# Kernel tuning notes

Hardware: AMD Instinct MI355X
Metric: run time of the kernel (lower is better)

The kernel has to match this reference:

```python
import jax, jax.numpy as jnp
import numpy as np

GRID = 7
COORD = 5.0
NO_OBJ = 0.5


def _corners(xywh, r, c):
    # xywh: [...,4] with (x_cell, y_cell, w, h); r,c broadcastable grid indices
    x, y, w, h = xywh[..., 0], xywh[..., 1], xywh[..., 2], xywh[..., 3]
    cx = (x + c) / GRID
    cy = (y + r) / GRID
    return cx - w / 2, cy - h / 2, cx + w / 2, cy + h / 2


def _iou(a, b):
    ax1, ay1, ax2, ay2 = a
    bx1, by1, bx2, by2 = b
    iw = jnp.maximum(jnp.minimum(ax2, bx2) - jnp.maximum(ax1, bx1), 0.0)
    ih = jnp.maximum(jnp.minimum(ay2, by2) - jnp.maximum(ay1, by1), 0.0)
    inter = iw * ih
    area_a = (ax2 - ax1) * (ay2 - ay1)
    area_b = (bx2 - bx1) * (by2 - by1)
    union = area_a + area_b - inter
    return jnp.where(union > 0, inter / jnp.where(union > 0, union, 1.0), 0.0)


def setup_inputs() -> dict:
    key = jax.random.key(0)
    k1, k2, k3 = jax.random.split(key, 3)
    B = 8192
    data = jax.random.uniform(k1, (B, GRID, GRID, 30), dtype=jnp.float32)
    labels = jax.random.uniform(k2, (B, GRID, GRID, 30), dtype=jnp.float32)
    # obj flag at channel 4 must be exactly 1 for obj cells
    obj = jax.random.randint(k3, (B, GRID, GRID), 0, 2).astype(jnp.float32)
    labels = labels.at[..., 4].set(obj)
    return {"data": data, "labels": labels}


def reference(data, labels):
    B = data.shape[0]
    r = jnp.arange(GRID, dtype=data.dtype)[None, :, None]  # row index -> y offset
    c = jnp.arange(GRID, dtype=data.dtype)[None, None, :]  # col index -> x offset

    box1 = _corners(data[..., 0:4], r, c)
    box2 = _corners(data[..., 5:9], r, c)
    gt = _corners(labels[..., 0:4], r, c)

    iou1 = _iou(box1, gt)  # [B,7,7]
    iou2 = _iou(box2, gt)
    resp1 = iou1 >= iou2

    xy1 = jnp.sum((data[..., 0:2] - labels[..., 0:2]) ** 2, -1)
    xy2 = jnp.sum((data[..., 5:7] - labels[..., 5:7]) ** 2, -1)
    wh1 = jnp.sum((jnp.sqrt(data[..., 2:4]) - jnp.sqrt(labels[..., 2:4])) ** 2, -1)
    wh2 = jnp.sum((jnp.sqrt(data[..., 7:9]) - jnp.sqrt(labels[..., 7:9])) ** 2, -1)

    d4, d9 = data[..., 4], data[..., 9]
    co = COORD * jnp.where(resp1, xy1, xy2)
    wh = COORD * jnp.where(resp1, wh1, wh2)
    confi = jnp.where(resp1, (d4 - iou1) ** 2, (d9 - iou2) ** 2)
    noobj_in = NO_OBJ * jnp.where(resp1, d9 ** 2, d4 ** 2)
    cls = jnp.sum((data[..., 10:] - labels[..., 10:]) ** 2, -1)

    m = (labels[..., 4] == 1).astype(data.dtype)
    obj_loss = m * (co + wh + confi + noobj_in + cls)
    noobj_loss = (1.0 - m) * NO_OBJ * (d4 ** 2 + d9 ** 2)
    return jnp.sum(obj_loss + noobj_loss) / B
```

## Files before the change

### kernel.cpp

```cpp
#include <hip/hip_runtime.h>

#define COORD 5.0f
#define NO_OBJ 0.5f
#define NCELLS (8192 * 49)
#define INV_B (1.0f / 8192.0f)

#define TPB 256
#define NBLK (NCELLS / TPB)

__device__ __forceinline__ float iou_calc(float ax1, float ay1, float ax2, float ay2,
                                          float bx1, float by1, float bx2, float by2) {
    float iw = fminf(ax2, bx2) - fmaxf(ax1, bx1);
    iw = fmaxf(iw, 0.0f);
    float ih = fminf(ay2, by2) - fmaxf(ay1, by1);
    ih = fmaxf(ih, 0.0f);
    float inter = iw * ih;
    float area_a = (ax2 - ax1) * (ay2 - ay1);
    float area_b = (bx2 - bx1) * (by2 - by1);
    float uni = area_a + area_b - inter;
    return uni > 0.0f ? inter / uni : 0.0f;
}

__global__ __launch_bounds__(TPB, 4) void yolo_loss_kernel(
    const float* __restrict__ data, const float* __restrict__ labels,
    float* __restrict__ ws) {
    const int tid = threadIdx.x;
    const int idx = blockIdx.x * TPB + tid;
    const int cell = idx % 49;
    const float r = (float)(cell / 7);
    const float c = (float)(cell % 7);

    float d[30], l[30];
    const float2* dp = (const float2*)(data + (size_t)idx * 30);
    const float2* lp = (const float2*)(labels + (size_t)idx * 30);
#pragma unroll
    for (int i = 0; i < 15; i++) {
        float2 v = dp[i];
        d[2 * i] = v.x; d[2 * i + 1] = v.y;
        float2 w2 = lp[i];
        l[2 * i] = w2.x; l[2 * i + 1] = w2.y;
    }

    const float inv_g = 1.0f / 7.0f;
    float cx1 = (d[0] + c) * inv_g, cy1 = (d[1] + r) * inv_g;
    float b1x1 = cx1 - d[2] * 0.5f, b1y1 = cy1 - d[3] * 0.5f;
    float b1x2 = cx1 + d[2] * 0.5f, b1y2 = cy1 + d[3] * 0.5f;
    float cx2 = (d[5] + c) * inv_g, cy2 = (d[6] + r) * inv_g;
    float b2x1 = cx2 - d[7] * 0.5f, b2y1 = cy2 - d[8] * 0.5f;
    float b2x2 = cx2 + d[7] * 0.5f, b2y2 = cy2 + d[8] * 0.5f;
    float gx = (l[0] + c) * inv_g, gy = (l[1] + r) * inv_g;
    float gx1 = gx - l[2] * 0.5f, gy1 = gy - l[3] * 0.5f;
    float gx2 = gx + l[2] * 0.5f, gy2 = gy + l[3] * 0.5f;

    float iou1 = iou_calc(b1x1, b1y1, b1x2, b1y2, gx1, gy1, gx2, gy2);
    float iou2 = iou_calc(b2x1, b2y1, b2x2, b2y2, gx1, gy1, gx2, gy2);
    bool resp1 = iou1 >= iou2;

    float xy1 = (d[0] - l[0]) * (d[0] - l[0]) + (d[1] - l[1]) * (d[1] - l[1]);
    float xy2 = (d[5] - l[5]) * (d[5] - l[5]) + (d[6] - l[6]) * (d[6] - l[6]);
    float s2 = sqrtf(d[2]) - sqrtf(l[2]);
    float s3 = sqrtf(d[3]) - sqrtf(l[3]);
    float wh1 = s2 * s2 + s3 * s3;
    float s7 = sqrtf(d[7]) - sqrtf(l[7]);
    float s8 = sqrtf(d[8]) - sqrtf(l[8]);
    float wh2 = s7 * s7 + s8 * s8;

    float d4 = d[4], d9 = d[9];
    float co = COORD * (resp1 ? xy1 : xy2);
    float wh = COORD * (resp1 ? wh1 : wh2);
    float ci = resp1 ? (d4 - iou1) * (d4 - iou1) : (d9 - iou2) * (d9 - iou2);
    float noobj_in = NO_OBJ * (resp1 ? d9 * d9 : d4 * d4);
    float cls = 0.0f;
#pragma unroll
    for (int i = 10; i < 30; i++) {
        float t = d[i] - l[i];
        cls += t * t;
    }

    float loss = (l[4] == 1.0f)
                     ? (co + wh + ci + noobj_in + cls)
                     : NO_OBJ * (d4 * d4 + d9 * d9);
    float acc = loss * INV_B;

#pragma unroll
    for (int off = 32; off > 0; off >>= 1)
        acc += __shfl_down(acc, off, 64);

    __shared__ float wsum[4];
    if ((tid & 63) == 0) wsum[tid >> 6] = acc;
    __syncthreads();
    if (tid == 0) ws[blockIdx.x] = wsum[0] + wsum[1] + wsum[2] + wsum[3];
}

__global__ __launch_bounds__(256) void reduce_kernel(const float* __restrict__ ws,
                                                     float* __restrict__ out) {
    float s = 0.0f;
    for (int i = threadIdx.x; i < NBLK; i += 256) s += ws[i];
#pragma unroll
    for (int off = 32; off > 0; off >>= 1)
        s += __shfl_down(s, off, 64);
    __shared__ float w[4];
    if ((threadIdx.x & 63) == 0) w[threadIdx.x >> 6] = s;
    __syncthreads();
    if (threadIdx.x == 0) out[0] = w[0] + w[1] + w[2] + w[3];
}

extern "C" void kernel_launch(void* const* d_in, const int* in_sizes, int n_in,
                              void* d_out, int out_size, void* d_ws, size_t ws_size,
                              hipStream_t stream) {
    const float* data = (const float*)d_in[0];
    const float* labels = (const float*)d_in[1];
    float* out = (float*)d_out;
    float* ws = (float*)d_ws;

    yolo_loss_kernel<<<NBLK, TPB, 0, stream>>>(data, labels, ws);
    reduce_kernel<<<1, 256, 0, stream>>>(ws, out);
}
```

Measured before the change: 119.3 us.

## Stage cell tiles into LDS with double-buffered global_load_lds in persistent blocks

Replaces the one-thread-per-cell kernel, which read each cell's 30 floats with strided float2 global loads. The new kernel uses 512 persistent blocks of 128 threads that copy contiguous 128-cell tiles of data and labels into LDS with async global_load_lds, double-buffered so the next tile loads while the current one is computed. The goal is fully coalesced global traffic and overlap of loading with compute. In exchange, each block now uses about 60KB of LDS, fewer waves are resident, and the LDS reads at a stride of 30 floats may hit bank conflicts.

```diff
diff --git a/kernel.cpp b/kernel.cpp
--- a/kernel.cpp
+++ b/kernel.cpp
@@ -5,8 +5,10 @@
 #define NCELLS (8192 * 49)
 #define INV_B (1.0f / 8192.0f)
 
-#define TPB 256
-#define NBLK (NCELLS / TPB)
+#define CPB 128
+#define FPT (CPB * 30)
+#define NTILES (NCELLS / CPB)
+#define NPBLK 512
 
 __device__ __forceinline__ float iou_calc(float ax1, float ay1, float ax2, float ay2,
                                           float bx1, float by1, float bx2, float by2) {
@@ -21,18 +23,31 @@
     return uni > 0.0f ? inter / uni : 0.0f;
 }
 
-__global__ __launch_bounds__(TPB, 4) void yolo_loss_kernel(
-    const float* __restrict__ data, const float* __restrict__ labels,
-    float* __restrict__ ws) {
-    const int tid = threadIdx.x;
-    const int idx = blockIdx.x * TPB + tid;
+__device__ __forceinline__ void stage_tile(const float* __restrict__ g, float* s, int tid) {
+#pragma unroll
+    for (int j = 0; j < 7; j++) {
+        __builtin_amdgcn_global_load_lds(
+            (const __attribute__((address_space(1))) void*)(g + j * 512 + tid * 4),
+            (__attribute__((address_space(3))) void*)(s + j * 512 + tid * 4), 16, 0, 0);
+    }
+#pragma unroll
+    for (int j = 0; j < 2; j++) {
+        __builtin_amdgcn_global_load_lds(
+            (const __attribute__((address_space(1))) void*)(g + 3584 + j * 128 + tid),
+            (__attribute__((address_space(3))) void*)(s + 3584 + j * 128 + tid), 4, 0, 0);
+    }
+}
+
+__device__ __forceinline__ float cell_loss(const float* __restrict__ sd,
+                                           const float* __restrict__ sl,
+                                           int idx, int tid) {
     const int cell = idx % 49;
     const float r = (float)(cell / 7);
     const float c = (float)(cell % 7);
 
     float d[30], l[30];
-    const float2* dp = (const float2*)(data + (size_t)idx * 30);
-    const float2* lp = (const float2*)(labels + (size_t)idx * 30);
+    const float2* dp = (const float2*)(sd + tid * 30);
+    const float2* lp = (const float2*)(sl + tid * 30);
 #pragma unroll
     for (int i = 0; i < 15; i++) {
         float2 v = dp[i];
@@ -77,25 +92,49 @@
         cls += t * t;
     }
 
-    float loss = (l[4] == 1.0f)
-                     ? (co + wh + ci + noobj_in + cls)
-                     : NO_OBJ * (d4 * d4 + d9 * d9);
-    float acc = loss * INV_B;
+    return (l[4] == 1.0f) ? (co + wh + ci + noobj_in + cls)
+                          : NO_OBJ * (d4 * d4 + d9 * d9);
+}
+
+__global__ __launch_bounds__(CPB) void yolo_loss_kernel(
+    const float* __restrict__ data, const float* __restrict__ labels,
+    float* __restrict__ ws) {
+    __shared__ float sd[2][FPT];
+    __shared__ float sl[2][FPT];
+
+    const int tid = threadIdx.x;
+    float acc = 0.0f;
+    int cur = 0;
+
+    stage_tile(data + (size_t)blockIdx.x * FPT, sd[0], tid);
+    stage_tile(labels + (size_t)blockIdx.x * FPT, sl[0], tid);
+
+    for (int i = blockIdx.x; i < NTILES; i += NPBLK) {
+        __syncthreads();
+        const int nxt = i + NPBLK;
+        if (nxt < NTILES) {
+            stage_tile(data + (size_t)nxt * FPT, sd[cur ^ 1], tid);
+            stage_tile(labels + (size_t)nxt * FPT, sl[cur ^ 1], tid);
+        }
+        acc += cell_loss(sd[cur], sl[cur], i * CPB + tid, tid);
+        cur ^= 1;
+    }
+    acc *= INV_B;
 
 #pragma unroll
     for (int off = 32; off > 0; off >>= 1)
         acc += __shfl_down(acc, off, 64);
 
-    __shared__ float wsum[4];
-    if ((tid & 63) == 0) wsum[tid >> 6] = acc;
     __syncthreads();
-    if (tid == 0) ws[blockIdx.x] = wsum[0] + wsum[1] + wsum[2] + wsum[3];
+    if ((tid & 63) == 0) sd[0][tid >> 6] = acc;
+    __syncthreads();
+    if (tid == 0) ws[blockIdx.x] = sd[0][0] + sd[0][1];
 }
 
 __global__ __launch_bounds__(256) void reduce_kernel(const float* __restrict__ ws,
                                                      float* __restrict__ out) {
     float s = 0.0f;
-    for (int i = threadIdx.x; i < NBLK; i += 256) s += ws[i];
+    for (int i = threadIdx.x; i < NPBLK; i += 256) s += ws[i];
 #pragma unroll
     for (int off = 32; off > 0; off >>= 1)
         s += __shfl_down(s, off, 64);
@@ -113,6 +152,6 @@
     float* out = (float*)d_out;
     float* ws = (float*)d_ws;
 
-    yolo_loss_kernel<<<NBLK, TPB, 0, stream>>>(data, labels, ws);
+    yolo_loss_kernel<<<NPBLK, CPB, 0, stream>>>(data, labels, ws);
     reduce_kernel<<<1, 256, 0, stream>>>(ws, out);
 }
```

Result: faster. 114.4 us (-4.1%).
